# Kernel optimization log

Hardware: AMD Instinct MI355X
Metric: run time of the kernel (lower is better)

## Reference

```python
import jax, jax.numpy as jnp
import numpy as np

N, C, H, W = 4, 256, 100, 100
COUT, G, EPS = 256, 32, 1e-5
K = 9  # 3x3 kernel positions

# regular 3x3 grid: row0 = dy, row1 = dx (mmcv offset convention)
REG = jnp.array([[-1,-1,-1,0,0,0,1,1,1],
                 [-1, 0, 1,-1,0,1,-1,0,1]], dtype=jnp.float32)  # (2,9)
KY = jnp.array([0,0,0,1,1,1,2,2,2], dtype=jnp.float32)
KX = jnp.array([0,1,2,0,1,2,0,1,2], dtype=jnp.float32)


def conv3x3(x, w, b):
    out = jax.lax.conv_general_dilated(x, w, window_strides=(1,1),
                                       padding=((1,1),(1,1)),
                                       dimension_numbers=('NCHW','OIHW','NCHW'))
    return out + b[None, :, None, None]


def setup_inputs() -> dict:
    key = jax.random.key(0)
    ks = jax.random.split(key, 7)
    x = jax.random.normal(ks[0], (N, C, H, W), dtype=jnp.float32)
    w_tm = jax.random.normal(ks[1], (4, C, 3, 3), dtype=jnp.float32) * 0.01
    b_tm = jnp.zeros((4,), dtype=jnp.float32)
    w_tr = jax.random.normal(ks[2], (2, C, 3, 3), dtype=jnp.float32) * 0.01
    b_tr = jnp.zeros((2,), dtype=jnp.float32)
    w_def = jax.random.normal(ks[3], (COUT, C, 3, 3), dtype=jnp.float32) * (1.0 / np.sqrt(C * 9.0))
    gn_w = 1.0 + 0.1 * jax.random.normal(ks[4], (COUT,), dtype=jnp.float32)
    gn_b = 0.1 * jax.random.normal(ks[5], (COUT,), dtype=jnp.float32)
    return dict(x=x, w_tm=w_tm, b_tm=b_tm, w_tr=w_tr, b_tr=b_tr,
                w_def=w_def, gn_w=gn_w, gn_b=gn_b)


def _compute_offsets(x, w_tm, b_tm, w_tr, b_tr):
    tm = conv3x3(x, w_tm, b_tm)                      # (N,4,H,W)
    tr = conv3x3(x, w_tr, b_tr)                      # (N,2,H,W)
    A = tm.transpose(0, 2, 3, 1).reshape(N, H, W, 2, 2)
    off = jnp.einsum('nhwij,jk->nhwik', A, REG) - REG  # (N,H,W,2,9)
    dy = (off[:, :, :, 0, :] + tr[:, 0][..., None]).transpose(0, 3, 1, 2)  # (N,9,H,W)
    dx = (off[:, :, :, 1, :] + tr[:, 1][..., None]).transpose(0, 3, 1, 2)
    return dy, dx


def _bilinear_sample(img, ys, xs):
    # img: (C,H,W); ys/xs: (9,H,W) float sampling coords; zero pad outside.
    y0 = jnp.floor(ys); x0 = jnp.floor(xs)
    wy = ys - y0; wx = xs - x0
    y0i = y0.astype(jnp.int32); x0i = x0.astype(jnp.int32)
    def gather(yi, xi):
        valid = (yi >= 0) & (yi < H) & (xi >= 0) & (xi < W)
        yc = jnp.clip(yi, 0, H - 1); xc = jnp.clip(xi, 0, W - 1)
        return img[:, yc, xc] * valid[None].astype(img.dtype)  # (C,9,H,W)
    v00 = gather(y0i,     x0i)
    v01 = gather(y0i,     x0i + 1)
    v10 = gather(y0i + 1, x0i)
    v11 = gather(y0i + 1, x0i + 1)
    return (v00 * (1 - wy) * (1 - wx) + v01 * (1 - wy) * wx
            + v10 * wy * (1 - wx) + v11 * wy * wx)


def _forward(x, w_tm, b_tm, w_tr, b_tr, w_def, gn_w, gn_b):
    dy, dx = _compute_offsets(x, w_tm, b_tm, w_tr, b_tr)
    # sampling positions: p*stride - pad + k*dil + offset  (stride=1, pad=dil=1)
    ys = jnp.arange(H, dtype=jnp.float32)[None, :, None] - 1.0 + KY[:, None, None] + dy
    xs = jnp.arange(W, dtype=jnp.float32)[None, None, :] - 1.0 + KX[:, None, None] + dx
    sampled = jax.vmap(_bilinear_sample)(x, ys, xs)       # (N,C,9,H,W)
    out = jnp.einsum('nckhw,ock->nohw', sampled, w_def.reshape(COUT, C, K))
    # GroupNorm(32) + ReLU
    g = out.reshape(N, G, (COUT // G) * H * W)
    mu = g.mean(axis=2, keepdims=True)
    var = g.var(axis=2, keepdims=True)
    g = (g - mu) * jax.lax.rsqrt(var + EPS)
    out = g.reshape(N, COUT, H, W) * gn_w[None, :, None, None] + gn_b[None, :, None, None]
    return jax.nn.relu(out)


def reference(x, w_tm, b_tm, w_tr, b_tr, w_def, gn_w, gn_b):
    return _forward(x, w_tm, b_tm, w_tr, b_tr, w_def, gn_w, gn_b)
```

## Files before the change

### kernel.cpp

```cpp
#include <hip/hip_runtime.h>
#include <math.h>

#define C_IN  256
#define HH    100
#define WW    100
#define HW    10000
#define NBAT  4
#define COUTC 256
#define K9    9
#define GG    32
#define TILES 13
#define NT2   169
#define EPSF  1e-5f

typedef _Float16 f16x8 __attribute__((ext_vector_type(8)));
typedef _Float16 h2v   __attribute__((ext_vector_type(2)));
typedef float    f32x4 __attribute__((ext_vector_type(4)));

__global__ void __launch_bounds__(256) k0_wfrag(const float* __restrict__ wd,
                                                _Float16* __restrict__ wf) {
  const int i = blockIdx.x * 256 + threadIdx.x;
  const int j  = i & 7;
  const int l  = (i >> 3) & 63;
  const int ot = (i >> 9) & 15;
  const int q  = i >> 13;
  const int tap = q >> 3, cg = q & 7;
  const int o = ot * 16 + (l & 15);
  const int c = cg * 32 + (l >> 4) * 8 + j;
  wf[i] = (_Float16)wd[((size_t)o * C_IN + c) * K9 + tap];
}

__global__ void __launch_bounds__(256) k0b_wfrag6(const float* __restrict__ w_tm,
                                                  const float* __restrict__ w_tr,
                                                  _Float16* __restrict__ wf) {
  const int i = blockIdx.x * 256 + threadIdx.x;
  const int j = i & 7, l = (i >> 3) & 63, q = i >> 9;
  const int tap = q >> 3, cg = q & 7;
  const int o = l & 15;
  const int c = cg * 32 + (l >> 4) * 8 + j;
  float v = 0.f;
  if (o < 4)      v = w_tm[((size_t)o * C_IN + c) * K9 + tap];
  else if (o < 6) v = w_tr[((size_t)(o - 4) * C_IN + c) * K9 + tap];
  wf[i] = (_Float16)v;
}

__global__ void __launch_bounds__(256) kt_nhwc(const float* __restrict__ x,
                                               _Float16* __restrict__ xh) {
  __shared__ float T[64][65];
  const int b = blockIdx.x;
  const int n = b / (4 * 157);
  const int r = b % (4 * 157);
  const int cg = r / 157, tile = r % 157;
  const int pbase = tile * 64, c0 = cg * 64;
  const int tid = threadIdx.x, lane = tid & 63, wv = tid >> 6;

#pragma unroll 4
  for (int i = 0; i < 16; ++i) {
    const int c = c0 + wv * 16 + i;
    const int pix = pbase + lane;
    T[wv * 16 + i][lane] = (pix < HW) ? x[((size_t)n * C_IN + c) * HW + pix] : 0.f;
  }
  __syncthreads();

  const int cl = tid & 15;
#pragma unroll
  for (int j = 0; j < 4; ++j) {
    const int pxl = (tid >> 4) + j * 16;
    const int pix = pbase + pxl;
    if (pix < HW) {
      const float v0 = T[cl * 4 + 0][pxl], v1 = T[cl * 4 + 1][pxl];
      const float v2 = T[cl * 4 + 2][pxl], v3 = T[cl * 4 + 3][pxl];
      uint2 pk;
      h2v a = {(_Float16)v0, (_Float16)v1};
      h2v bq = {(_Float16)v2, (_Float16)v3};
      pk.x = __builtin_bit_cast(unsigned, a);
      pk.y = __builtin_bit_cast(unsigned, bq);
      *(uint2*)(xh + ((size_t)n * HW + pix) * C_IN + c0 + cl * 4) = pk;
    }
  }
}

#define RAW_BARRIER()                                                         \
  asm volatile("s_waitcnt lgkmcnt(0)" ::: "memory");                          \
  __builtin_amdgcn_sched_barrier(0);                                          \
  __builtin_amdgcn_s_barrier();                                               \
  __builtin_amdgcn_sched_barrier(0);

__global__ void __launch_bounds__(256) k1_off(
    const _Float16* __restrict__ xh, const _Float16* __restrict__ wf6,
    const float* __restrict__ b_tm, const float* __restrict__ b_tr,
    float* __restrict__ posy, float* __restrict__ posx) {
  const int tid = threadIdx.x, lane = tid & 63, wv = tid >> 6;
  const int s = blockIdx.x * 4 + wv;
  const int n = s / 625, strip = s % 625;
  const int ps = strip * 16;
  const int px = ps + (lane & 15);
  const int h = px / WW, w = px % WW;
  const char* xbase = (const char*)(xh + (size_t)n * HW * C_IN) + (lane >> 4) * 16;

  int nbA, nbB; bool vA, vB;
#define K1NB(T_, NB, V)                                                       \
  { const int y = h + (T_) / 3 - 1, xx = w + (T_) % 3 - 1;                    \
    V = ((unsigned)y < (unsigned)HH) && ((unsigned)xx < (unsigned)WW);        \
    NB = (V ? (y * WW + xx) : 0) * 512; }

  uint4 q0, q1, q2, q3;
  K1NB(0, nbA, vA)
  nbB = nbA; vB = vA;
  q0 = *(const uint4*)(xbase + nbA + 0 * 64);
  q1 = *(const uint4*)(xbase + nbA + 1 * 64);
  q2 = *(const uint4*)(xbase + nbA + 2 * 64);
  q3 = *(const uint4*)(xbase + nbA + 3 * 64);
  f16x8 afA = *(const f16x8*)(wf6 + (size_t)0 * 512 + lane * 8);
  f16x8 afB = *(const f16x8*)(wf6 + (size_t)1 * 512 + lane * 8);

  f32x4 acc = (f32x4)(0.f);
  const uint4 z4 = {0u, 0u, 0u, 0u};

#define K1SUB(CG, Q, AF)                                                      \
  {                                                                           \
    const int p = t * 8 + (CG);                                               \
    uint4 bq = vA ? Q : z4;                                                   \
    f16x8 bf = __builtin_bit_cast(f16x8, bq);                                 \
    if ((CG) == 2) { K1NB((t < 8 ? t + 1 : 8), nbB, vB) }                     \
    if ((CG) < 4) { Q = *(const uint4*)(xbase + nbA + ((CG) + 4) * 64); }     \
    else if (t < 8) { Q = *(const uint4*)(xbase + nbB + ((CG) - 4) * 64); }   \
    acc = __builtin_amdgcn_mfma_f32_16x16x32_f16(AF, bf, acc, 0, 0, 0);       \
    if ((CG) < 6 || t < 8)                                                    \
      AF = *(const f16x8*)(wf6 + (size_t)(p + 2) * 512 + lane * 8);           \
  }

  for (int t = 0; t < 9; ++t) {
    K1SUB(0, q0, afA) K1SUB(1, q1, afB) K1SUB(2, q2, afA) K1SUB(3, q3, afB)
    K1SUB(4, q0, afA) K1SUB(5, q1, afB) K1SUB(6, q2, afA) K1SUB(7, q3, afB)
    nbA = nbB; vA = vB;
  }

  const float t0v = __shfl(acc[0], (lane & 15) + 16);
  const float t1v = __shfl(acc[1], (lane & 15) + 16);
  if (lane < 16) {
    const float A00 = acc[0] + b_tm[0], A01 = acc[1] + b_tm[1];
    const float A10 = acc[2] + b_tm[2], A11 = acc[3] + b_tm[3];
    const float t0 = t0v + b_tr[0], t1 = t1v + b_tr[1];
    const float fh = (float)h, fw = (float)w;
#pragma unroll
    for (int k = 0; k < 9; ++k) {
      const float ry = (float)(k / 3 - 1);
      const float rx = (float)(k % 3 - 1);
      posy[((size_t)n * K9 + k) * HW + px] = fh + t0 + A00 * ry + A01 * rx;
      posx[((size_t)n * K9 + k) * HW + px] = fw + t1 + A10 * ry + A11 * rx;
    }
  }
}

__global__ void __launch_bounds__(512, 4) k2_deform(
    const _Float16* __restrict__ xh, const _Float16* __restrict__ wfrag,
    const float* __restrict__ posy, const float* __restrict__ posx,
    float* __restrict__ out, float* __restrict__ part, int* __restrict__ qcnt) {
  __shared__ __align__(16) char Bs[2 * 2 * 64 * 64];
  __shared__ __align__(16) unsigned int ctab[576 * 8];
  __shared__ int s_tile;

  const int tid = threadIdx.x, lane = tid & 63, wv = tid >> 6;
  const int px_s = tid >> 3, oct = tid & 7;
  const int chunkpar = oct >> 2, qo = oct & 3;
  const int wsw = (((qo + (px_s >> 1)) & 3) << 4);
  const int rpx = lane & 15, rko = lane >> 4;
  const int rsw = (((rko + (rpx >> 1)) & 3) << 4);

  for (;;) {
    __syncthreads();
    if (tid == 0) s_tile = atomicAdd(qcnt, 1);
    __syncthreads();
    const int wg = s_tile;
    if (wg >= NBAT * NT2) break;
    const int n = wg / NT2, rem = wg % NT2;
    const int ty = rem / TILES, tx = rem % TILES;

    for (int s = tid; s < 576; s += 512) {
      const int tap = s >> 6, j = s & 63;
      const int row = ty * 8 + (j >> 3), col = tx * 8 + (j & 7);
      const bool pvv = (row < HH) && (col < WW);
      const int mpa = pvv ? (row * WW + col) : 0;
      float ys = posy[((size_t)n * K9 + tap) * HW + mpa];
      float xs = posx[((size_t)n * K9 + tap) * HW + mpa];
      if (!pvv) { ys = -1e4f; xs = -1e4f; }
      const float y0f = floorf(ys), x0f = floorf(xs);
      const float wy = ys - y0f, wx = xs - x0f;
      const int iy0 = (int)y0f, ix0 = (int)x0f;
      const bool vy0 = ((unsigned)iy0 < (unsigned)HH);
      const bool vy1 = ((unsigned)(iy0 + 1) < (unsigned)HH);
      const bool vx0 = ((unsigned)ix0 < (unsigned)WW);
      const bool vx1 = ((unsigned)(ix0 + 1) < (unsigned)WW);
      const bool v0 = vy0 && vx0, v1 = vy0 && vx1;
      const bool v2 = vy1 && vx0, v3 = vy1 && vx1;
      uint4 oa, wa;
      oa.x = (v0 ? (iy0 * WW + ix0) : 0) * 512u;
      oa.y = (v1 ? (iy0 * WW + ix0 + 1) : 0) * 512u;
      oa.z = (v2 ? ((iy0 + 1) * WW + ix0) : 0) * 512u;
      oa.w = (v3 ? ((iy0 + 1) * WW + ix0 + 1) : 0) * 512u;
      const float g0 = v0 ? (1.f - wy) * (1.f - wx) : 0.f;
      const float g1 = v1 ? (1.f - wy) * wx : 0.f;
      const float g2 = v2 ? wy * (1.f - wx) : 0.f;
      const float g3 = v3 ? wy * wx : 0.f;
      const _Float16 h0 = (_Float16)g0, h1 = (_Float16)g1;
      const _Float16 h2_ = (_Float16)g2, h3 = (_Float16)g3;
      wa.x = __builtin_bit_cast(unsigned, (h2v){h0, h0});
      wa.y = __builtin_bit_cast(unsigned, (h2v){h1, h1});
      wa.z = __builtin_bit_cast(unsigned, (h2v){h2_, h2_});
      wa.w = __builtin_bit_cast(unsigned, (h2v){h3, h3});
      uint4* cp = (uint4*)&ctab[s * 8];
      cp[0] = oa;
      cp[1] = wa;
    }
    __syncthreads();

    const char* xbase = (const char*)(xh + (size_t)n * HW * C_IN);

    uint4 O, Wt, c0, c1, c2, c3;
    f16x8 aA0, aA1, aB0, aB1;

#define ISSUE(G)                                                              \
  {                                                                           \
    const uint4* ce = (const uint4*)&ctab[(((G) >> 2) * 64 + px_s) * 8];      \
    O = ce[0];                                                                \
    Wt = ce[1];                                                               \
    const int choff = ((G) & 3) * 128 + oct * 16;                             \
    c0 = *(const uint4*)(xbase + O.x + choff);                                \
    c1 = *(const uint4*)(xbase + O.y + choff);                                \
    c2 = *(const uint4*)(xbase + O.z + choff);                                \
    c3 = *(const uint4*)(xbase + O.w + choff);                                \
  }

#define CW1(c)                                                                \
  __builtin_bit_cast(unsigned,                                                \
      (h2v)(w0 * __builtin_bit_cast(h2v, c0.c) +                              \
            w1 * __builtin_bit_cast(h2v, c1.c) +                              \
            w2 * __builtin_bit_cast(h2v, c2.c) +                              \
            w3 * __builtin_bit_cast(h2v, c3.c)))

#define COMBINE_WRITE(BUFW)                                                   \
  {                                                                           \
    h2v w0 = __builtin_bit_cast(h2v, Wt.x), w1 = __builtin_bit_cast(h2v, Wt.y); \
    h2v w2 = __builtin_bit_cast(h2v, Wt.z), w3 = __builtin_bit_cast(h2v, Wt.w); \
    uint4 sv;                                                                 \
    sv.x = CW1(x);                                                            \
    sv.y = CW1(y);                                                            \
    sv.z = CW1(z);                                                            \
    sv.w = CW1(w);                                                            \
    *(uint4*)(Bs + (BUFW) * 8192 + chunkpar * 4096 + px_s * 64 + wsw) = sv;   \
  }

#define LOADA(A0_, A1_, CK)                                                   \
  {                                                                           \
    const _Float16* wfp = wfrag + (((size_t)(CK) * 16 + wv * 2) * 64 + lane) * 8; \
    A0_ = *(const f16x8*)(wfp);                                               \
    A1_ = *(const f16x8*)(wfp + 512);                                         \
  }

    f32x4 acc[2][4];
#pragma unroll
    for (int ot = 0; ot < 2; ++ot)
#pragma unroll
      for (int bt = 0; bt < 4; ++bt) acc[ot][bt] = (f32x4)(0.f);

#define MF(a, bx, o_, b_) \
  acc[o_][b_] = __builtin_amdgcn_mfma_f32_16x16x32_f16(a, bx, acc[o_][b_], 0, 0, 0);

#define MFMA8(A0_, A1_, BUF, CP)                                              \
  {                                                                           \
    const char* bb = Bs + (BUF) * 8192 + (CP) * 4096 + rpx * 64 + rsw;        \
    f16x8 b0 = *(const f16x8*)(bb);                                           \
    f16x8 b1 = *(const f16x8*)(bb + 1024);                                    \
    f16x8 b2 = *(const f16x8*)(bb + 2048);                                    \
    f16x8 b3 = *(const f16x8*)(bb + 3072);                                    \
    __builtin_amdgcn_s_setprio(1);                                            \
    MF(A0_, b0, 0, 0) MF(A1_, b0, 1, 0)                                       \
    MF(A0_, b1, 0, 1) MF(A1_, b1, 1, 1)                                       \
    MF(A0_, b2, 0, 2) MF(A1_, b2, 1, 2)                                       \
    MF(A0_, b3, 0, 3) MF(A1_, b3, 1, 3)                                       \
    __builtin_amdgcn_s_setprio(0);                                            \
  }

#define GSEC(G, BUF)                                                          \
  {                                                                           \
    MFMA8(aA0, aA1, BUF, 0)                                                   \
    LOADA(aA0, aA1, 2 * ((G) + 1))                                            \
    MFMA8(aB0, aB1, BUF, 1)                                                   \
    LOADA(aB0, aB1, 2 * ((G) + 1) + 1)                                        \
    COMBINE_WRITE((BUF) ^ 1)                                                  \
    ISSUE((G) + 2)                                                            \
    RAW_BARRIER()                                                             \
  }

    ISSUE(0)
    COMBINE_WRITE(0)
    ISSUE(1)
    LOADA(aA0, aA1, 0)
    LOADA(aB0, aB1, 1)
    RAW_BARRIER()

    for (int gp = 0; gp < 17; ++gp) {
      GSEC(2 * gp, 0)
      GSEC(2 * gp + 1, 1)
    }
    MFMA8(aA0, aA1, 0, 0)
    LOADA(aA0, aA1, 70)
    MFMA8(aB0, aB1, 0, 1)
    LOADA(aB0, aB1, 71)
    COMBINE_WRITE(1)
    RAW_BARRIER()
    MFMA8(aA0, aA1, 1, 0)
    MFMA8(aB0, aB1, 1, 1)

    float* grA = (float*)Bs;
    float* grB = grA + 1024;
    const int colb = lane & 15, prow = (lane >> 4) * 4;
#pragma unroll
    for (int ot = 0; ot < 2; ++ot) {
      float s1 = 0.f, s2 = 0.f;
#pragma unroll
      for (int bt = 0; bt < 4; ++bt) {
        const int jj = bt * 16 + colb;
        const int row = ty * 8 + (jj >> 3), col = tx * 8 + (jj & 7);
        const f32x4 a = acc[ot][bt];
        if (row < HH && col < WW) {
          float* op = out + ((size_t)(n * COUTC + wv * 32 + ot * 16 + prow)) * HW +
                      row * WW + col;
          op[0] = a[0];
          op[HW] = a[1];
          op[2 * HW] = a[2];
          op[3 * HW] = a[3];
        }
        s1 += a[0] + a[1] + a[2] + a[3];
        s2 += a[0] * a[0] + a[1] * a[1] + a[2] * a[2] + a[3] * a[3];
      }
      grA[(wv * 2 + ot) * 64 + lane] = s1;
      grB[(wv * 2 + ot) * 64 + lane] = s2;
    }
    __syncthreads();
    if (tid < 32) {
      const int wv2 = tid >> 2, ot2 = (tid >> 1) & 1, hb = tid & 1;
      float a1 = 0.f, a2 = 0.f;
#pragma unroll 8
      for (int l = 0; l < 32; ++l) {
        a1 += grA[(wv2 * 2 + ot2) * 64 + hb * 32 + l];
        a2 += grB[(wv2 * 2 + ot2) * 64 + hb * 32 + l];
      }
      float* pp = part + (((size_t)n * NT2 + rem) * GG + tid) * 2;
      pp[0] = a1;
      pp[1] = a2;
    }
  }
}

__global__ void __launch_bounds__(64) k3_stats(const float* __restrict__ part,
                                               float* __restrict__ stats) {
  const int b = blockIdx.x;
  const int n = b >> 5, g = b & 31;
  double s = 0.0, q = 0.0;
  for (int i = threadIdx.x; i < NT2; i += 64) {
    const float* pp = part + (((size_t)n * NT2 + i) * GG + g) * 2;
    s += pp[0];
    q += pp[1];
  }
#pragma unroll
  for (int off = 32; off > 0; off >>= 1) {
    s += __shfl_down(s, off);
    q += __shfl_down(q, off);
  }
  if (threadIdx.x == 0) {
    const double cnt = 8.0 * (double)HW;
    const double mean = s / cnt;
    const double var = q / cnt - mean * mean;
    stats[b * 2 + 0] = (float)mean;
    stats[b * 2 + 1] = (float)(1.0 / sqrt(var + (double)EPSF));
  }
}

__global__ void __launch_bounds__(256) k4_norm(float* __restrict__ out,
                                               const float* __restrict__ stats,
                                               const float* __restrict__ gw,
                                               const float* __restrict__ gb) {
  const size_t i4 = (size_t)blockIdx.x * 256 + threadIdx.x;
  const size_t idx = i4 * 4;
  const int n = (int)(idx / ((size_t)COUTC * HW));
  const int r = (int)(idx % ((size_t)COUTC * HW));
  const int o = r / HW;
  const int g = o >> 3;
  const float mean = stats[(n * GG + g) * 2 + 0];
  const float rs = stats[(n * GG + g) * 2 + 1];
  const float sc = rs * gw[o];
  const float sh = gb[o] - mean * sc;
  float4 v = *(float4*)(out + idx);
  v.x = fmaxf(fmaf(v.x, sc, sh), 0.f);
  v.y = fmaxf(fmaf(v.y, sc, sh), 0.f);
  v.z = fmaxf(fmaf(v.z, sc, sh), 0.f);
  v.w = fmaxf(fmaf(v.w, sc, sh), 0.f);
  *(float4*)(out + idx) = v;
}

extern "C" void kernel_launch(void* const* d_in, const int* in_sizes, int n_in,
                              void* d_out, int out_size, void* d_ws, size_t ws_size,
                              hipStream_t stream) {
  const float* x    = (const float*)d_in[0];
  const float* w_tm = (const float*)d_in[1];
  const float* b_tm = (const float*)d_in[2];
  const float* w_tr = (const float*)d_in[3];
  const float* b_tr = (const float*)d_in[4];
  const float* w_def = (const float*)d_in[5];
  const float* gn_w = (const float*)d_in[6];
  const float* gn_b = (const float*)d_in[7];
  float* out = (float*)d_out;
  float* ws = (float*)d_ws;

  float* posy  = ws;
  float* posx  = ws + 360000;
  _Float16* wfrag = (_Float16*)(ws + 720000);
  _Float16* wf6   = (_Float16*)(ws + 1014912);
  _Float16* xh    = (_Float16*)(ws + 1033344);
  float* part  = ws + 6153344;
  float* stats = ws + 6236544;
  int* qcnt    = (int*)(ws + 6236800);

  hipMemsetAsync(qcnt, 0, sizeof(int), stream);
  hipLaunchKernelGGL(k0_wfrag, dim3(2304), dim3(256), 0, stream, w_def, wfrag);
  hipLaunchKernelGGL(k0b_wfrag6, dim3(144), dim3(256), 0, stream, w_tm, w_tr, wf6);
  hipLaunchKernelGGL(kt_nhwc, dim3(2512), dim3(256), 0, stream, x, xh);
  hipLaunchKernelGGL(k1_off, dim3(625), dim3(256), 0, stream,
                     xh, wf6, b_tm, b_tr, posy, posx);
  hipLaunchKernelGGL(k2_deform, dim3(512), dim3(512), 0, stream,
                     xh, wfrag, posy, posx, out, part, qcnt);
  hipLaunchKernelGGL(k3_stats, dim3(NBAT * GG), dim3(64), 0, stream, part, stats);
  hipLaunchKernelGGL(k4_norm, dim3(10000), dim3(256), 0, stream,
                     out, stats, gn_w, gn_b);
}
```

Measured before the change: 154.5 us.

## Halve deform block to 4 waves, each computing 64 output channels

The deformable-conv kernel drops from 512 to 256 threads per block. Each wave now computes 64 output channels (4 A-fragments, 16 MFMAs per step) instead of 32, so every bilinearly sampled B tile in LDS feeds twice as many MFMAs. The K loop becomes 72 single-chunk steps of 64 channels with half-size double buffers. The change cuts sampling/combine work per MFMA and LDS footprint, at the cost of more accumulator and A-fragment registers (launch bounds 256,3) and possibly lower occupancy or less latency hiding for the gathers.

```diff
diff --git a/kernel.cpp b/kernel.cpp
--- a/kernel.cpp
+++ b/kernel.cpp
@@ -153,17 +153,16 @@
   }
 }
 
-__global__ void __launch_bounds__(512, 4) k2_deform(
+__global__ void __launch_bounds__(256, 3) k2_deform(
     const _Float16* __restrict__ xh, const _Float16* __restrict__ wfrag,
     const float* __restrict__ posy, const float* __restrict__ posx,
     float* __restrict__ out, float* __restrict__ part, int* __restrict__ qcnt) {
-  __shared__ __align__(16) char Bs[2 * 2 * 64 * 64];
+  __shared__ __align__(16) char Bs[2 * 64 * 64];
   __shared__ __align__(16) unsigned int ctab[576 * 8];
   __shared__ int s_tile;
 
   const int tid = threadIdx.x, lane = tid & 63, wv = tid >> 6;
-  const int px_s = tid >> 3, oct = tid & 7;
-  const int chunkpar = oct >> 2, qo = oct & 3;
+  const int px_s = tid >> 2, qo = tid & 3;
   const int wsw = (((qo + (px_s >> 1)) & 3) << 4);
   const int rpx = lane & 15, rko = lane >> 4;
   const int rsw = (((rko + (rpx >> 1)) & 3) << 4);
@@ -177,7 +176,7 @@
     const int n = wg / NT2, rem = wg % NT2;
     const int ty = rem / TILES, tx = rem % TILES;
 
-    for (int s = tid; s < 576; s += 512) {
+    for (int s = tid; s < 576; s += 256) {
       const int tap = s >> 6, j = s & 63;
       const int row = ty * 8 + (j >> 3), col = tx * 8 + (j & 7);
       const bool pvv = (row < HH) && (col < WW);
@@ -218,14 +217,14 @@
     const char* xbase = (const char*)(xh + (size_t)n * HW * C_IN);
 
     uint4 O, Wt, c0, c1, c2, c3;
-    f16x8 aA0, aA1, aB0, aB1;
-
-#define ISSUE(G)                                                              \
+    f16x8 aA0, aA1, aA2, aA3, aB0, aB1, aB2, aB3;
+
+#define ISSUE(S)                                                              \
   {                                                                           \
-    const uint4* ce = (const uint4*)&ctab[(((G) >> 2) * 64 + px_s) * 8];      \
+    const uint4* ce = (const uint4*)&ctab[((((S) >> 3)) * 64 + px_s) * 8];    \
     O = ce[0];                                                                \
     Wt = ce[1];                                                               \
-    const int choff = ((G) & 3) * 128 + oct * 16;                             \
+    const int choff = ((S) & 7) * 64 + qo * 16;                               \
     c0 = *(const uint4*)(xbase + O.x + choff);                                \
     c1 = *(const uint4*)(xbase + O.y + choff);                                \
     c2 = *(const uint4*)(xbase + O.z + choff);                                \
@@ -248,84 +247,80 @@
     sv.y = CW1(y);                                                            \
     sv.z = CW1(z);                                                            \
     sv.w = CW1(w);                                                            \
-    *(uint4*)(Bs + (BUFW) * 8192 + chunkpar * 4096 + px_s * 64 + wsw) = sv;   \
-  }
-
-#define LOADA(A0_, A1_, CK)                                                   \
+    *(uint4*)(Bs + (BUFW) * 4096 + px_s * 64 + wsw) = sv;                     \
+  }
+
+#define LOADA4(A0_, A1_, A2_, A3_, CK)                                        \
   {                                                                           \
-    const _Float16* wfp = wfrag + (((size_t)(CK) * 16 + wv * 2) * 64 + lane) * 8; \
+    const _Float16* wfp = wfrag + (((size_t)(CK) * 16 + wv * 4) * 64 + lane) * 8; \
     A0_ = *(const f16x8*)(wfp);                                               \
     A1_ = *(const f16x8*)(wfp + 512);                                         \
-  }
-
-    f32x4 acc[2][4];
-#pragma unroll
-    for (int ot = 0; ot < 2; ++ot)
-#pragma unroll
-      for (int bt = 0; bt < 4; ++bt) acc[ot][bt] = (f32x4)(0.f);
-
-#define MF(a, bx, o_, b_) \
-  acc[o_][b_] = __builtin_amdgcn_mfma_f32_16x16x32_f16(a, bx, acc[o_][b_], 0, 0, 0);
-
-#define MFMA8(A0_, A1_, BUF, CP)                                              \
+    A2_ = *(const f16x8*)(wfp + 1024);                                        \
+    A3_ = *(const f16x8*)(wfp + 1536);                                        \
+  }
+
+    f32x4 acc[4][4];
+#pragma unroll
+    for (int tt = 0; tt < 4; ++tt)
+#pragma unroll
+      for (int bt = 0; bt < 4; ++bt) acc[tt][bt] = (f32x4)(0.f);
+
+#define MF(a, bx, t_, b_) \
+  acc[t_][b_] = __builtin_amdgcn_mfma_f32_16x16x32_f16(a, bx, acc[t_][b_], 0, 0, 0);
+
+#define MFMA16(A0_, A1_, A2_, A3_, BUF)                                       \
   {                                                                           \
-    const char* bb = Bs + (BUF) * 8192 + (CP) * 4096 + rpx * 64 + rsw;        \
+    const char* bb = Bs + (BUF) * 4096 + rpx * 64 + rsw;                      \
     f16x8 b0 = *(const f16x8*)(bb);                                           \
     f16x8 b1 = *(const f16x8*)(bb + 1024);                                    \
     f16x8 b2 = *(const f16x8*)(bb + 2048);                                    \
     f16x8 b3 = *(const f16x8*)(bb + 3072);                                    \
     __builtin_amdgcn_s_setprio(1);                                            \
-    MF(A0_, b0, 0, 0) MF(A1_, b0, 1, 0)                                       \
-    MF(A0_, b1, 0, 1) MF(A1_, b1, 1, 1)                                       \
-    MF(A0_, b2, 0, 2) MF(A1_, b2, 1, 2)                                       \
-    MF(A0_, b3, 0, 3) MF(A1_, b3, 1, 3)                                       \
+    MF(A0_, b0, 0, 0) MF(A1_, b0, 1, 0) MF(A2_, b0, 2, 0) MF(A3_, b0, 3, 0)   \
+    MF(A0_, b1, 0, 1) MF(A1_, b1, 1, 1) MF(A2_, b1, 2, 1) MF(A3_, b1, 3, 1)   \
+    MF(A0_, b2, 0, 2) MF(A1_, b2, 1, 2) MF(A2_, b2, 2, 2) MF(A3_, b2, 3, 2)   \
+    MF(A0_, b3, 0, 3) MF(A1_, b3, 1, 3) MF(A2_, b3, 2, 3) MF(A3_, b3, 3, 3)   \
     __builtin_amdgcn_s_setprio(0);                                            \
-  }
-
-#define GSEC(G, BUF)                                                          \
-  {                                                                           \
-    MFMA8(aA0, aA1, BUF, 0)                                                   \
-    LOADA(aA0, aA1, 2 * ((G) + 1))                                            \
-    MFMA8(aB0, aB1, BUF, 1)                                                   \
-    LOADA(aB0, aB1, 2 * ((G) + 1) + 1)                                        \
-    COMBINE_WRITE((BUF) ^ 1)                                                  \
-    ISSUE((G) + 2)                                                            \
-    RAW_BARRIER()                                                             \
   }
 
     ISSUE(0)
     COMBINE_WRITE(0)
     ISSUE(1)
-    LOADA(aA0, aA1, 0)
-    LOADA(aB0, aB1, 1)
+    LOADA4(aA0, aA1, aA2, aA3, 0)
+    LOADA4(aB0, aB1, aB2, aB3, 1)
     RAW_BARRIER()
 
-    for (int gp = 0; gp < 17; ++gp) {
-      GSEC(2 * gp, 0)
-      GSEC(2 * gp + 1, 1)
-    }
-    MFMA8(aA0, aA1, 0, 0)
-    LOADA(aA0, aA1, 70)
-    MFMA8(aB0, aB1, 0, 1)
-    LOADA(aB0, aB1, 71)
+    for (int sp = 0; sp < 35; ++sp) {
+      const int s0 = 2 * sp, s1 = 2 * sp + 1;
+      MFMA16(aA0, aA1, aA2, aA3, 0)
+      LOADA4(aA0, aA1, aA2, aA3, s0 + 2)
+      COMBINE_WRITE(1)
+      ISSUE(s0 + 2)
+      RAW_BARRIER()
+      MFMA16(aB0, aB1, aB2, aB3, 1)
+      LOADA4(aB0, aB1, aB2, aB3, s1 + 2)
+      COMBINE_WRITE(0)
+      ISSUE(s1 + 2)
+      RAW_BARRIER()
+    }
+    MFMA16(aA0, aA1, aA2, aA3, 0)
     COMBINE_WRITE(1)
     RAW_BARRIER()
-    MFMA8(aA0, aA1, 1, 0)
-    MFMA8(aB0, aB1, 1, 1)
-
-    float* grA = (float*)Bs;
+    MFMA16(aB0, aB1, aB2, aB3, 1)
+
+    float* grA = (float*)ctab;
     float* grB = grA + 1024;
     const int colb = lane & 15, prow = (lane >> 4) * 4;
 #pragma unroll
-    for (int ot = 0; ot < 2; ++ot) {
+    for (int tt = 0; tt < 4; ++tt) {
       float s1 = 0.f, s2 = 0.f;
 #pragma unroll
       for (int bt = 0; bt < 4; ++bt) {
         const int jj = bt * 16 + colb;
         const int row = ty * 8 + (jj >> 3), col = tx * 8 + (jj & 7);
-        const f32x4 a = acc[ot][bt];
+        const f32x4 a = acc[tt][bt];
         if (row < HH && col < WW) {
-          float* op = out + ((size_t)(n * COUTC + wv * 32 + ot * 16 + prow)) * HW +
+          float* op = out + ((size_t)(n * COUTC + wv * 64 + tt * 16 + prow)) * HW +
                       row * WW + col;
           op[0] = a[0];
           op[HW] = a[1];
@@ -335,17 +330,17 @@
         s1 += a[0] + a[1] + a[2] + a[3];
         s2 += a[0] * a[0] + a[1] * a[1] + a[2] * a[2] + a[3] * a[3];
       }
-      grA[(wv * 2 + ot) * 64 + lane] = s1;
-      grB[(wv * 2 + ot) * 64 + lane] = s2;
+      grA[(wv * 4 + tt) * 64 + lane] = s1;
+      grB[(wv * 4 + tt) * 64 + lane] = s2;
     }
     __syncthreads();
     if (tid < 32) {
-      const int wv2 = tid >> 2, ot2 = (tid >> 1) & 1, hb = tid & 1;
+      const int wv2 = tid >> 3, tt2 = (tid >> 1) & 3, bit = tid & 1;
       float a1 = 0.f, a2 = 0.f;
 #pragma unroll 8
       for (int l = 0; l < 32; ++l) {
-        a1 += grA[(wv2 * 2 + ot2) * 64 + hb * 32 + l];
-        a2 += grB[(wv2 * 2 + ot2) * 64 + hb * 32 + l];
+        a1 += grA[(wv2 * 4 + tt2) * 64 + bit * 32 + l];
+        a2 += grB[(wv2 * 4 + tt2) * 64 + bit * 32 + l];
       }
       float* pp = part + (((size_t)n * NT2 + rem) * GG + tid) * 2;
       pp[0] = a1;
@@ -429,7 +424,7 @@
   hipLaunchKernelGGL(kt_nhwc, dim3(2512), dim3(256), 0, stream, x, xh);
   hipLaunchKernelGGL(k1_off, dim3(625), dim3(256), 0, stream,
                      xh, wf6, b_tm, b_tr, posy, posx);
-  hipLaunchKernelGGL(k2_deform, dim3(512), dim3(512), 0, stream,
+  hipLaunchKernelGGL(k2_deform, dim3(768), dim3(256), 0, stream,
                      xh, wfrag, posy, posx, out, part, qcnt);
   hipLaunchKernelGGL(k3_stats, dim3(NBAT * GG), dim3(64), 0, stream, part, stats);
   hipLaunchKernelGGL(k4_norm, dim3(10000), dim3(256), 0, stream,
```

Result: slower. 165.0 us (+6.8%).
